# Kernel tuning notes

Hardware: AMD Instinct MI355X
Metric: run time of the kernel (lower is better)

The kernel has to match this reference:

```python
import jax, jax.numpy as jnp
import numpy as np

DIM_X, DIM_Y, DIM_D, DIM_H = 100, 1, 100, 256
T = 1.0


def setup_inputs() -> dict:
    key = jax.random.key(0)
    ks = jax.random.split(key, 10)
    B, N = 2048, 128

    def lin(k, fi, fo):
        # kaiming-ish scaling so the relu MLP stays well-conditioned
        return (jax.random.normal(k, (fi, fo), jnp.float32) / np.sqrt(fi)).astype(jnp.float32)

    return {
        "W_noise": jax.random.normal(ks[0], (B, DIM_D, N), jnp.float32),  # unscaled randn; *sqrt(dt) in reference
        "signs": jax.random.randint(ks[1], (N,), 0, 2).astype(jnp.int32),  # 0/1 -> mapped to +-1
        "x0": jnp.ones((DIM_X,), jnp.float32),
        "y0": jax.random.uniform(ks[2], (DIM_Y,), jnp.float32),
        "Wi": lin(ks[3], DIM_X + 1, DIM_H),
        "bi": jnp.zeros((DIM_H,), jnp.float32),
        "Wh1": lin(ks[4], DIM_H, DIM_H),
        "bh1": jnp.zeros((DIM_H,), jnp.float32),
        "Wh2": lin(ks[5], DIM_H, DIM_H),
        "bh2": jnp.zeros((DIM_H,), jnp.float32),
        "Wo": lin(ks[6], DIM_H, DIM_Y * DIM_D),
        "bo": jnp.zeros((DIM_Y * DIM_D,), jnp.float32),
        "batch_size": B,
        "N": N,
    }


def reference(W_noise, signs, x0, y0, Wi, bi, Wh1, bh1, Wh2, bh2, Wo, bo, batch_size, N):
    dt = jnp.float32(T / N)
    sqdt = jnp.sqrt(dt)
    sqrt2 = jnp.sqrt(jnp.float32(2.0))
    B = W_noise.shape[0]

    W = W_noise * sqdt                                   # Brownian increments [B, D, N]
    s_pm = (2 * signs - 1).astype(jnp.float32)           # +-1 per step
    ones_col = jnp.ones((B, 1), jnp.float32)

    def phi(u):  # relu MLP -> [B, dim_y, dim_d]
        h = jax.nn.relu(u @ Wi + bi)
        h = jax.nn.relu(h @ Wh1 + bh1)
        h = jax.nn.relu(h @ Wh2 + bh2)
        return (h @ Wo + bo).reshape(-1, DIM_Y, DIM_D)

    def f_fn(t, x, y, z):  # driver f(t,x,y,z) = ||z||^2 over d
        return jnp.sum(z * z, axis=-1)  # [B, dim_y]

    x_init = x0 + jnp.zeros((B, DIM_X), jnp.float32)
    y_init = y0 + jnp.zeros((B, DIM_Y), jnp.float32)

    xs = (jnp.moveaxis(W, 2, 0), s_pm, jnp.arange(N, dtype=jnp.float32))

    def step(carry, inp):
        x, y = carry
        w, s, i = inp                      # w: [B, D]
        t0 = dt * i
        t1 = dt * (i + 1.0)
        sdt = s * sqdt
        z = phi(jnp.concatenate([x, ones_col * t0], axis=1))
        # b = 0, sigma = sqrt(2)*I  =>  matmul(sigma, w -+ S*sqrt(dt)) = sqrt(2)*(w -+ sdt)
        k1 = sqrt2 * (w - sdt)
        k2 = sqrt2 * (w + sdt)
        y1 = -f_fn(t0, x, y, z) * dt + jnp.einsum('byd,bd->by', z, w - sdt)
        z_new = phi(jnp.concatenate([x + k1, ones_col * t1], axis=1))
        y2 = -f_fn(t1, x, y + y1, z) * dt + jnp.einsum('byd,bd->by', z_new, w + sdt)
        return (x + 0.5 * (k1 + k2), y + 0.5 * (y1 + y2)), None

    (x, y), _ = jax.lax.scan(step, (x_init, y_init), xs)
    return x, y
```

## Files before the change

### kernel.cpp

```cpp
#include <hip/hip_runtime.h>
#include <hip/hip_bf16.h>

typedef __hip_bfloat16 bf16;
typedef __attribute__((ext_vector_type(8))) short bf16x8v;
typedef __attribute__((ext_vector_type(4))) float f32x4;
typedef __attribute__((ext_vector_type(4))) short short4v;

#define B_SZ   2048
#define NSTEP  128
#define DD     100
#define DX     100
#define DH     256

#define UCOLS  104

__device__ __constant__ const float DT_   = 0.0078125f;
__device__ __constant__ const float SQDT_ = 0.08838834764831845f;
__device__ __constant__ const float C1_   = 0.125f;

__global__ __launch_bounds__(128) void prep_kernel(
    const float* __restrict__ Wn, const int* __restrict__ signs,
    const float* __restrict__ x0,
    bf16* __restrict__ U, float* __restrict__ xout)
{
    __shared__ float w_l[DD * 129];
    __shared__ float s_l[NSTEP];
    const int b = blockIdx.x, tid = threadIdx.x;
    const float* wb = Wn + (size_t)b * DD * NSTEP;

    for (int idx = tid; idx < DD * NSTEP; idx += 128) {
        int d = idx >> 7, i = idx & 127;
        w_l[d * 129 + i] = wb[idx];
    }
    if (tid < NSTEP) s_l[tid] = 2.f * (float)signs[tid] - 1.f;
    __syncthreads();

    if (tid < DD) {
        const int d = tid;
        float x = x0[d];
        for (int i = 0; i < NSTEP; ++i) {
            size_t p = ((size_t)(b * NSTEP + i)) * 2;
            float wn = w_l[d * 129 + i];
            U[p * UCOLS + d]       = __float2bfloat16(x);
            U[(p + 1) * UCOLS + d] = __float2bfloat16(x + C1_ * (wn - s_l[i]));
            x += C1_ * wn;
        }
        xout[(size_t)b * DX + d] = x;
    } else if (tid < UCOLS) {
        for (int i = 0; i < NSTEP; ++i) {
            size_t p = ((size_t)(b * NSTEP + i)) * 2;
            float v0 = 0.f, v1 = 0.f;
            if (tid == 100) { v0 = DT_ * (float)i; v1 = DT_ * (float)(i + 1); }
            U[p * UCOLS + tid]       = __float2bfloat16(v0);
            U[(p + 1) * UCOLS + tid] = __float2bfloat16(v1);
        }
    }
}

__global__ __launch_bounds__(256) void wpack_kernel(
    const float* __restrict__ W, bf16* __restrict__ dst,
    int Kact, int Nact, int KC, int total)
{
    int idx = blockIdx.x * 256 + threadIdx.x;
    if (idx >= total) return;
    int j = idx & 7;
    int l = (idx >> 3) & 63;
    int c = (idx >> 9) % KC;
    int t = idx / (KC * 512);
    int n = t * 16 + (l & 15);
    int k = c * 32 + (l >> 4) * 8 + j;
    float v = (k < Kact && n < Nact) ? W[(size_t)k * Nact + n] : 0.f;
    dst[idx] = __float2bfloat16(v);
}

__global__ __launch_bounds__(256) void bpack_kernel(
    const float* __restrict__ bi, const float* __restrict__ bh1,
    const float* __restrict__ bh2, const float* __restrict__ bo,
    float* __restrict__ dst)
{
    int i = blockIdx.x * 256 + threadIdx.x;
    if (i < 256) dst[i] = bi[i];
    else if (i < 512) dst[i] = bh1[i - 256];
    else if (i < 768) dst[i] = bh2[i - 512];
    else if (i < 896) dst[i] = (i - 768 < DD) ? bo[i - 768] : 0.f;
}

template<int KC, int NT, int MT, int SRC_STRIDE, int DST_STRIDE, bool RELU>
__device__ __forceinline__ void layer_ip(
    char* __restrict__ buf,
    const bf16* __restrict__ wfrag, const float* __restrict__ bias,
    int lane, int w)
{
    const int lrow = lane & 15;
    const int lkg  = lane >> 4;
    f32x4 acc[NT][MT];
#pragma unroll
    for (int t = 0; t < NT; ++t)
#pragma unroll
        for (int mt = 0; mt < MT; ++mt) acc[t][mt] = (f32x4){0.f, 0.f, 0.f, 0.f};

    const char* wptr = (const char*)wfrag + ((size_t)(w * NT) * KC * 64 + lane) * 16;

    bf16x8v a_cur[NT];
#pragma unroll
    for (int t = 0; t < NT; ++t)
        a_cur[t] = *(const bf16x8v*)(wptr + (size_t)(t * KC) * 1024);

#pragma unroll
    for (int c = 0; c < KC; ++c) {
        bf16x8v b[MT];
#pragma unroll
        for (int mt = 0; mt < MT; ++mt) {
            int m = mt * 16 + lrow;
            b[mt] = *(const bf16x8v*)(buf + m * SRC_STRIDE +
                                      ((c * 64 + lkg * 16) ^ ((m & 7) << 4)));
        }
        bf16x8v a_nxt[NT];
        if (c + 1 < KC) {
#pragma unroll
            for (int t = 0; t < NT; ++t)
                a_nxt[t] = *(const bf16x8v*)(wptr + (size_t)(t * KC + c + 1) * 1024);
        }
        __builtin_amdgcn_s_setprio(1);
#pragma unroll
        for (int t = 0; t < NT; ++t)
#pragma unroll
            for (int mt = 0; mt < MT; ++mt)
                acc[t][mt] = __builtin_amdgcn_mfma_f32_16x16x32_bf16(a_cur[t], b[mt], acc[t][mt], 0, 0, 0);
        __builtin_amdgcn_s_setprio(0);
        if (c + 1 < KC) {
#pragma unroll
            for (int t = 0; t < NT; ++t) a_cur[t] = a_nxt[t];
        }
    }

    __syncthreads();

#pragma unroll
    for (int t = 0; t < NT; ++t) {
        const int nb = (w * NT + t) * 16 + lkg * 4;
        const float4 bv = *(const float4*)(bias + nb);
#pragma unroll
        for (int mt = 0; mt < MT; ++mt) {
            const int m = mt * 16 + lrow;
            float v0 = acc[t][mt][0] + bv.x;
            float v1 = acc[t][mt][1] + bv.y;
            float v2 = acc[t][mt][2] + bv.z;
            float v3 = acc[t][mt][3] + bv.w;
            if (RELU) {
                v0 = fmaxf(v0, 0.f); v1 = fmaxf(v1, 0.f);
                v2 = fmaxf(v2, 0.f); v3 = fmaxf(v3, 0.f);
            }
            bf16 h0 = __float2bfloat16(v0), h1 = __float2bfloat16(v1);
            bf16 h2 = __float2bfloat16(v2), h3 = __float2bfloat16(v3);
            short4v pv;
            pv[0] = *(short*)&h0; pv[1] = *(short*)&h1;
            pv[2] = *(short*)&h2; pv[3] = *(short*)&h3;
            *(short4v*)(buf + m * DST_STRIDE + ((nb * 2) ^ ((m & 7) << 4))) = pv;
        }
    }
}

__global__ __launch_bounds__(256, 2) void mlp_mfma_kernel(
    const bf16* __restrict__ U,
    const float* __restrict__ Wn, const int* __restrict__ signs,
    const bf16* __restrict__ wfWi, const bf16* __restrict__ wfWh1,
    const bf16* __restrict__ wfWh2, const bf16* __restrict__ wfWo,
    const float* __restrict__ biases, float* __restrict__ incr)
{
    __shared__ char buf[128 * 512];
    __shared__ float Sz2[128], Szw[128];
    const int tid = threadIdx.x;
    const int lane = tid & 63, w = tid >> 6;
    const size_t row0 = (size_t)blockIdx.x * 128;

    {
        const char* usrc = (const char*)(U + row0 * UCOLS);
        for (int idx = tid; idx < 2048; idx += 256) {
            int r = idx >> 4, c = idx & 15;
            uint4 v = (uint4){0, 0, 0, 0};
            if (c < 13) v = *(const uint4*)(usrc + r * 208 + c * 16);
            *(uint4*)(buf + r * 256 + ((c * 16) ^ ((r & 7) << 4))) = v;
        }
    }
    __syncthreads();

    layer_ip<4, 4, 8, 256, 512, true >(buf, wfWi,  biases,        lane, w);
    __syncthreads();
    layer_ip<8, 4, 8, 512, 512, true >(buf, wfWh1, biases + 256,  lane, w);
    __syncthreads();
    layer_ip<8, 4, 8, 512, 512, true >(buf, wfWh2, biases + 512,  lane, w);
    __syncthreads();
    layer_ip<8, 2, 8, 512, 256, false>(buf, wfWo,  biases + 768,  lane, w);
    __syncthreads();

    const int q = tid & 3;
#pragma unroll
    for (int half = 0; half < 2; ++half) {
        const int r = (tid >> 2) + half * 64;
        const size_t g = row0 + r;
        const size_t pair = g >> 1;
        const int h = (int)(g & 1);
        const int bb = (int)(pair >> 7), ii = (int)(pair & 127);
        const float s = 2.f * (float)signs[ii] - 1.f;
        const float sdt = s * SQDT_;
        const float* wb = Wn + (size_t)bb * DD * NSTEP + ii;

        float sz2 = 0.f, szw = 0.f;
        for (int d = q; d < DD; d += 4) {
            unsigned short zb = *(const unsigned short*)(buf + r * 256 + ((d * 2) ^ ((r & 7) << 4)));
            union { unsigned int u; float f; } cv; cv.u = ((unsigned int)zb) << 16;
            float z = cv.f;
            float wv = SQDT_ * wb[(size_t)d * NSTEP];
            float wt = h ? (wv + sdt) : (wv - sdt);
            sz2 += z * z;
            szw += z * wt;
        }
        sz2 += __shfl_xor(sz2, 1); sz2 += __shfl_xor(sz2, 2);
        szw += __shfl_xor(szw, 1); szw += __shfl_xor(szw, 2);
        if (q == 0) { Sz2[r] = sz2; Szw[r] = szw; }
    }
    __syncthreads();

    if (tid < 64) {
        int rr = tid * 2;
        incr[row0 / 2 + tid] = -Sz2[rr] * DT_ + 0.5f * (Szw[rr] + Szw[rr + 1]);
    }
}

__global__ __launch_bounds__(128) void y_kernel(
    const float* __restrict__ incr, const float* __restrict__ y0,
    float* __restrict__ yout)
{
    const int b = blockIdx.x, tid = threadIdx.x;
    float v = incr[(size_t)b * NSTEP + tid];
#pragma unroll
    for (int off = 1; off < 64; off <<= 1) v += __shfl_xor(v, off);
    __shared__ float partial[2];
    if ((tid & 63) == 0) partial[tid >> 6] = v;
    __syncthreads();
    if (tid == 0) yout[b] = y0[0] + partial[0] + partial[1];
}

extern "C" void kernel_launch(void* const* d_in, const int* in_sizes, int n_in,
                              void* d_out, int out_size, void* d_ws, size_t ws_size,
                              hipStream_t stream) {
    (void)in_sizes; (void)n_in; (void)out_size; (void)ws_size;
    const float* Wn    = (const float*)d_in[0];
    const int*   signs = (const int*)d_in[1];
    const float* x0    = (const float*)d_in[2];
    const float* y0    = (const float*)d_in[3];
    const float* Wi    = (const float*)d_in[4];
    const float* bi    = (const float*)d_in[5];
    const float* Wh1   = (const float*)d_in[6];
    const float* bh1   = (const float*)d_in[7];
    const float* Wh2   = (const float*)d_in[8];
    const float* bh2   = (const float*)d_in[9];
    const float* Wo    = (const float*)d_in[10];
    const float* bo    = (const float*)d_in[11];

    float* out  = (float*)d_out;
    float* xout = out;
    float* yout = out + (size_t)B_SZ * DX;

    const size_t NROWS = (size_t)B_SZ * NSTEP * 2;
    char* ws = (char*)d_ws;
    size_t off = 0;
    bf16*  U      = (bf16*)(ws + off); off += NROWS * UCOLS * sizeof(bf16);
    float* incr   = (float*)(ws + off); off += (NROWS / 2) * sizeof(float);
    bf16*  wfWi   = (bf16*)(ws + off); off += 32768 * sizeof(bf16);
    bf16*  wfWh1  = (bf16*)(ws + off); off += 65536 * sizeof(bf16);
    bf16*  wfWh2  = (bf16*)(ws + off); off += 65536 * sizeof(bf16);
    bf16*  wfWo   = (bf16*)(ws + off); off += 32768 * sizeof(bf16);
    float* biases = (float*)(ws + off); off += 896 * sizeof(float);

    prep_kernel<<<B_SZ, 128, 0, stream>>>(Wn, signs, x0, U, xout);
    wpack_kernel<<<128, 256, 0, stream>>>(Wi,  wfWi,  101, 256, 4, 32768);
    wpack_kernel<<<256, 256, 0, stream>>>(Wh1, wfWh1, 256, 256, 8, 65536);
    wpack_kernel<<<256, 256, 0, stream>>>(Wh2, wfWh2, 256, 256, 8, 65536);
    wpack_kernel<<<128, 256, 0, stream>>>(Wo,  wfWo,  256, 100, 8, 32768);
    bpack_kernel<<<4, 256, 0, stream>>>(bi, bh1, bh2, bo, biases);

    mlp_mfma_kernel<<<(int)(NROWS / 128), 256, 0, stream>>>(
        U, Wn, signs, wfWi, wfWh1, wfWh2, wfWo, biases, incr);
    y_kernel<<<B_SZ, 128, 0, stream>>>(incr, y0, yout);
}
```

Measured before the change: 320.8 us.

## Tile MLP layers 2x2 across warps and drop register prefetch of weight fragments

Each layer was split so every warp covered all 128 rows and a quarter of the output columns. It is now split into a 2x2 warp grid, with each warp covering 64 rows and half the columns (NT doubled, MT halved). This halves each warp's LDS activation reads but doubles its global weight-fragment loads. The explicit double-buffered prefetch of weight fragments is also removed; weights are now loaded inline just before their MFMAs, which lowers register pressure but may expose global-load latency.

```diff
diff --git a/kernel.cpp b/kernel.cpp
--- a/kernel.cpp
+++ b/kernel.cpp
@@ -89,7 +89,7 @@
 __device__ __forceinline__ void layer_ip(
     char* __restrict__ buf,
     const bf16* __restrict__ wfrag, const float* __restrict__ bias,
-    int lane, int w)
+    int lane, int m0, int nt0)
 {
     const int lrow = lane & 15;
     const int lkg  = lane >> 4;
@@ -99,50 +99,37 @@
 #pragma unroll
         for (int mt = 0; mt < MT; ++mt) acc[t][mt] = (f32x4){0.f, 0.f, 0.f, 0.f};
 
-    const char* wptr = (const char*)wfrag + ((size_t)(w * NT) * KC * 64 + lane) * 16;
-
-    bf16x8v a_cur[NT];
-#pragma unroll
-    for (int t = 0; t < NT; ++t)
-        a_cur[t] = *(const bf16x8v*)(wptr + (size_t)(t * KC) * 1024);
+    const char* wptr = (const char*)wfrag + ((size_t)nt0 * KC * 64 + lane) * 16;
 
 #pragma unroll
     for (int c = 0; c < KC; ++c) {
         bf16x8v b[MT];
 #pragma unroll
         for (int mt = 0; mt < MT; ++mt) {
-            int m = mt * 16 + lrow;
+            int m = m0 + mt * 16 + lrow;
             b[mt] = *(const bf16x8v*)(buf + m * SRC_STRIDE +
                                       ((c * 64 + lkg * 16) ^ ((m & 7) << 4)));
         }
-        bf16x8v a_nxt[NT];
-        if (c + 1 < KC) {
-#pragma unroll
-            for (int t = 0; t < NT; ++t)
-                a_nxt[t] = *(const bf16x8v*)(wptr + (size_t)(t * KC + c + 1) * 1024);
-        }
         __builtin_amdgcn_s_setprio(1);
 #pragma unroll
-        for (int t = 0; t < NT; ++t)
+        for (int t = 0; t < NT; ++t) {
+            bf16x8v a = *(const bf16x8v*)(wptr + (size_t)(t * KC + c) * 1024);
 #pragma unroll
             for (int mt = 0; mt < MT; ++mt)
-                acc[t][mt] = __builtin_amdgcn_mfma_f32_16x16x32_bf16(a_cur[t], b[mt], acc[t][mt], 0, 0, 0);
+                acc[t][mt] = __builtin_amdgcn_mfma_f32_16x16x32_bf16(a, b[mt], acc[t][mt], 0, 0, 0);
+        }
         __builtin_amdgcn_s_setprio(0);
-        if (c + 1 < KC) {
-#pragma unroll
-            for (int t = 0; t < NT; ++t) a_cur[t] = a_nxt[t];
-        }
     }
 
     __syncthreads();
 
 #pragma unroll
     for (int t = 0; t < NT; ++t) {
-        const int nb = (w * NT + t) * 16 + lkg * 4;
+        const int nb = (nt0 + t) * 16 + lkg * 4;
         const float4 bv = *(const float4*)(bias + nb);
 #pragma unroll
         for (int mt = 0; mt < MT; ++mt) {
-            const int m = mt * 16 + lrow;
+            const int m = m0 + mt * 16 + lrow;
             float v0 = acc[t][mt][0] + bv.x;
             float v1 = acc[t][mt][1] + bv.y;
             float v2 = acc[t][mt][2] + bv.z;
@@ -172,6 +159,8 @@
     __shared__ float Sz2[128], Szw[128];
     const int tid = threadIdx.x;
     const int lane = tid & 63, w = tid >> 6;
+    const int wm = w >> 1, wn = w & 1;
+    const int m0 = wm * 64;
     const size_t row0 = (size_t)blockIdx.x * 128;
 
     {
@@ -185,13 +174,13 @@
     }
     __syncthreads();
 
-    layer_ip<4, 4, 8, 256, 512, true >(buf, wfWi,  biases,        lane, w);
-    __syncthreads();
-    layer_ip<8, 4, 8, 512, 512, true >(buf, wfWh1, biases + 256,  lane, w);
-    __syncthreads();
-    layer_ip<8, 4, 8, 512, 512, true >(buf, wfWh2, biases + 512,  lane, w);
-    __syncthreads();
-    layer_ip<8, 2, 8, 512, 256, false>(buf, wfWo,  biases + 768,  lane, w);
+    layer_ip<4, 8, 4, 256, 512, true >(buf, wfWi,  biases,        lane, m0, wn * 8);
+    __syncthreads();
+    layer_ip<8, 8, 4, 512, 512, true >(buf, wfWh1, biases + 256,  lane, m0, wn * 8);
+    __syncthreads();
+    layer_ip<8, 8, 4, 512, 512, true >(buf, wfWh2, biases + 512,  lane, m0, wn * 8);
+    __syncthreads();
+    layer_ip<8, 4, 4, 512, 256, false>(buf, wfWo,  biases + 768,  lane, m0, wn * 4);
     __syncthreads();
 
     const int q = tid & 3;
```

New measurement: 480.5 us. 1.5x slower.
